# Performance work log

Hardware: AMD Instinct MI355X
Metric: run time of the kernel (lower is better)

The kernel has to match this reference:

```python
import jax, jax.numpy as jnp
import numpy as np

INTER = 256
TEMPERATURE = 4.0
NEG_FILL = -1e9


def setup_inputs() -> dict:
    key = jax.random.key(0)
    ks = jax.random.split(key, 8)
    B, C, H, W = 8, 512, 64, 64
    x_query = jax.random.normal(ks[0], (B, C, H, W), dtype=jnp.float32)
    x_support = jax.random.normal(ks[1], (B, C, H, W), dtype=jnp.float32)
    support_embedding = jax.random.normal(ks[2], (B, INTER, H, W), dtype=jnp.float32)
    support_mask = jax.random.randint(ks[3], (B, 1, H, W), 0, 2).astype(jnp.float32)
    scale = 1.0 / np.sqrt(C)
    theta_w = jax.random.normal(ks[4], (INTER, C), dtype=jnp.float32) * scale
    theta_b = jax.random.normal(ks[5], (INTER,), dtype=jnp.float32) * 0.01
    phi_w = jax.random.normal(ks[6], (INTER, C), dtype=jnp.float32) * scale
    phi_b = jax.random.normal(ks[7], (INTER,), dtype=jnp.float32) * 0.01
    return {
        "x_query": x_query,
        "x_support": x_support,
        "support_embedding": support_embedding,
        "support_mask": support_mask,
        "theta_w": theta_w,
        "theta_b": theta_b,
        "phi_w": phi_w,
        "phi_b": phi_b,
    }


def reference(x_query, x_support, support_embedding, support_mask, theta_w, theta_b, phi_w, phi_b):
    B, C, H, W = x_query.shape
    N = H * W
    # g_x: [B, N, 256]
    g_x = support_embedding.reshape(B, INTER, N).transpose(0, 2, 1)
    # 1x1 convs == per-pixel linear over channels
    theta_x = jnp.einsum('oc,bcn->bno', theta_w, x_query.reshape(B, C, N)) + theta_b  # [B, N, 256]
    phi_x = jnp.einsum('oc,bcn->bon', phi_w, x_support.reshape(B, C, N)) + phi_b[None, :, None]  # [B, 256, N]
    f = jnp.matmul(theta_x, phi_x)  # [B, N, N]
    mask = support_mask.reshape(B, 1, N)
    f = f * mask
    # equality-based mask fill (matches torch masked_fill(f == 0, -1e9))
    f = jnp.where(f == 0, NEG_FILL, f) / TEMPERATURE
    attn = jax.nn.softmax(f, axis=-1)  # dropout is identity in eval mode
    y = jnp.matmul(attn, g_x)  # [B, N, 256]
    y = y.transpose(0, 2, 1).reshape(B, INTER, H, W)
    return y
```

## Files before the change

kernel.cpp:

```cpp
#include <hip/hip_runtime.h>
#include <hip/hip_fp16.h>
#include <stdint.h>

typedef _Float16 f16x8 __attribute__((ext_vector_type(8)));
typedef _Float16 f16x4 __attribute__((ext_vector_type(4)));
typedef float    f32x4 __attribute__((ext_vector_type(4)));

#define MFMA16(a, b, c) __builtin_amdgcn_mfma_f32_16x16x32_f16(a, b, c, 0, 0, 0)

static constexpr int BN   = 8;
static constexpr int CIN  = 512;
static constexpr int NHW  = 4096;
static constexpr int OD   = 256;
static constexpr int KBLK = 32;

#define RSWZ(row, cb) ((((row) << 7)) + ((cb) ^ (((row) & 7) << 4)))

__device__ __forceinline__ f16x8 cvt8(const float4 a, const float4 b) {
    f16x8 r;
    r[0] = (_Float16)a.x; r[1] = (_Float16)a.y; r[2] = (_Float16)a.z; r[3] = (_Float16)a.w;
    r[4] = (_Float16)b.x; r[5] = (_Float16)b.y; r[6] = (_Float16)b.z; r[7] = (_Float16)b.w;
    return r;
}

__device__ __forceinline__ uint32_t pkh2(float x, float y) {
    union { _Float16 h[2]; uint32_t u; } z;
    z.h[0] = (_Float16)x; z.h[1] = (_Float16)y;
    return z.u;
}

__global__ __launch_bounds__(256)
void setup(const float* __restrict__ thw, const float* __restrict__ phw,
           _Float16* __restrict__ wf,
           const float* __restrict__ mask, int* __restrict__ idx,
           int* __restrict__ pos, int* __restrict__ nbArr)
{
    __shared__ int cnt[256];
    __shared__ int pre[257];
    const int t = threadIdx.x;

    if (blockIdx.x < 128) {
        const int i = blockIdx.x * 256 + t;
        const float4 a = ((const float4*)thw)[i];
        const float4 b = ((const float4*)phw)[i];
        f16x4 ra, rb;
        ra[0] = (_Float16)a.x; ra[1] = (_Float16)a.y; ra[2] = (_Float16)a.z; ra[3] = (_Float16)a.w;
        rb[0] = (_Float16)b.x; rb[1] = (_Float16)b.y; rb[2] = (_Float16)b.z; rb[3] = (_Float16)b.w;
        *(f16x4*)(wf + (size_t)i * 4)          = ra;
        *(f16x4*)(wf + 131072 + (size_t)i * 4) = rb;
        return;
    }

    const int b = blockIdx.x - 128;
    const float* mb = mask + (size_t)b * NHW;
    const int base = t * 16;
    float mv[16];
    int c = 0;
    #pragma unroll
    for (int i = 0; i < 16; ++i) { mv[i] = mb[base + i]; c += (mv[i] != 0.0f); }
    cnt[t] = c;
    __syncthreads();
    if (t == 0) {
        int s = 0;
        for (int i = 0; i < 256; ++i) { pre[i] = s; s += cnt[i]; }
        pre[256] = s;
    }
    __syncthreads();
    int o = pre[t];
    #pragma unroll
    for (int i = 0; i < 16; ++i) {
        if (mv[i] != 0.0f) {
            idx[(size_t)b * NHW + o] = base + i;
            pos[(size_t)b * NHW + base + i] = o;
            ++o;
        } else {
            pos[(size_t)b * NHW + base + i] = -1;
        }
    }
    const int Nb = pre[256];
    const int Npad = (Nb + 63) & ~63;
    for (int k = Nb + t; k < Npad; k += 256) idx[(size_t)b * NHW + k] = 0;
    if (t == 0) { nbArr[b * 2] = Nb; nbArr[b * 2 + 1] = Npad >> 5; }
}

__global__ __launch_bounds__(256)
void prep_gather(const float* __restrict__ xq, const float* __restrict__ xs,
                 const _Float16* __restrict__ wf,
                 const float* __restrict__ thb, const float* __restrict__ phb,
                 const int* __restrict__ pos,
                 const float* __restrict__ emb, const int* __restrict__ idx,
                 const int* __restrict__ nbArr,
                 _Float16* __restrict__ Qws, _Float16* __restrict__ Kc,
                 _Float16* __restrict__ Vc)
{
    __shared__ __align__(16) char Xs[64 * 128];
    __shared__ __align__(16) char Ws[256 * 128];
    __shared__ int Ps[64];
    __shared__ int sidx[64];

    const int t    = threadIdx.x;
    const int z    = blockIdx.y;

    if (z >= 16) {
        const int b = z - 16, k0 = blockIdx.x * 64;
        const int Nb = nbArr[b * 2];
        const int Npad = (Nb + 63) & ~63;
        if (k0 >= Npad) return;
        if (t < 64) sidx[t] = idx[(size_t)b * NHW + k0 + t];
        __syncthreads();
        const float* eb = emb + (size_t)b * OD * NHW;
        char* VcB = (char*)(Vc + (size_t)b * OD * NHW);
        #pragma unroll
        for (int r = 0; r < 8; ++r) {
            const int u = r * 256 + t;
            const int o = u >> 3, uc = u & 7;
            const int chunk = uc >> 2, uin = uc & 3;
            float4 a, c;
            #pragma unroll
            for (int i = 0; i < 4; ++i) ((float*)&a)[i] = eb[(size_t)o * NHW + sidx[uc * 8 + i]];
            #pragma unroll
            for (int i = 0; i < 4; ++i) ((float*)&c)[i] = eb[(size_t)o * NHW + sidx[uc * 8 + 4 + i]];
            const f16x8 v = cvt8(a, c);
            *(f16x8*)(VcB + (size_t)o * (NHW * 2) + (size_t)k0 * 2 + chunk * 64
                          + ((uin ^ ((o >> 1) & 3)) * 16)) = v;
        }
        return;
    }

    const int nt = blockIdx.x;
    const int b = z >> 1, sel = z & 1;
    const float* x        = (sel ? xs : xq) + (size_t)b * CIN * NHW;
    const _Float16* w     = wf + (size_t)sel * (OD * CIN);
    const float* bias     = sel ? phb : thb;
    const int n0 = nt * 64;

    const int lane = t & 63, wave = t >> 6;
    const int l16  = lane & 15, lh = lane >> 4;

    if (sel && t < 64) Ps[t] = pos[(size_t)b * NHW + n0 + t];

    f32x4 acc[4][4] = {};

    for (int c0 = 0; c0 < CIN; c0 += 64) {
        #pragma unroll
        for (int rep = 0; rep < 4; ++rep) {
            const int ci = rep * 16 + (t >> 4);
            const int nl = (t & 15) * 4;
            const float4 v = *(const float4*)&x[(size_t)(c0 + ci) * NHW + n0 + nl];
            *(_Float16*)(Xs + RSWZ(nl + 0, ci * 2)) = (_Float16)v.x;
            *(_Float16*)(Xs + RSWZ(nl + 1, ci * 2)) = (_Float16)v.y;
            *(_Float16*)(Xs + RSWZ(nl + 2, ci * 2)) = (_Float16)v.z;
            *(_Float16*)(Xs + RSWZ(nl + 3, ci * 2)) = (_Float16)v.w;
        }
        #pragma unroll
        for (int r = 0; r < 8; ++r) {
            const int u = r * 256 + t;
            const int o = u >> 3, cs8 = (u & 7) * 8;
            const f16x8 v = *(const f16x8*)(w + (size_t)o * CIN + c0 + cs8);
            *(f16x8*)(Ws + RSWZ(o, cs8 * 2)) = v;
        }
        __syncthreads();

        #pragma unroll
        for (int kk = 0; kk < 2; ++kk) {
            f16x8 af[4];
            #pragma unroll
            for (int oo = 0; oo < 4; ++oo)
                af[oo] = *(const f16x8*)(Ws + RSWZ(wave * 64 + oo * 16 + l16, kk * 64 + lh * 16));
            #pragma unroll
            for (int nn = 0; nn < 4; ++nn) {
                const f16x8 bf = *(const f16x8*)(Xs + RSWZ(nn * 16 + l16, kk * 64 + lh * 16));
                #pragma unroll
                for (int oo = 0; oo < 4; ++oo)
                    acc[oo][nn] = MFMA16(af[oo], bf, acc[oo][nn]);
            }
        }
        __syncthreads();
    }

    if (!sel) {
        _Float16* out = Qws + (size_t)b * NHW * OD;
        #pragma unroll
        for (int oo = 0; oo < 4; ++oo) {
            const float4 bi = *(const float4*)&bias[wave * 64 + oo * 16 + lh * 4];
            #pragma unroll
            for (int nn = 0; nn < 4; ++nn) {
                f16x4 v;
                v[0] = (_Float16)(acc[oo][nn][0] + bi.x);
                v[1] = (_Float16)(acc[oo][nn][1] + bi.y);
                v[2] = (_Float16)(acc[oo][nn][2] + bi.z);
                v[3] = (_Float16)(acc[oo][nn][3] + bi.w);
                const int n = n0 + nn * 16 + l16;
                *(f16x4*)&out[(size_t)n * OD + wave * 64 + oo * 16 + lh * 4] = v;
            }
        }
    } else {
        char* KcB = (char*)(Kc + (size_t)b * NHW * OD);
        #pragma unroll
        for (int oo = 0; oo < 4; ++oo) {
            const float4 bi = *(const float4*)&bias[wave * 64 + oo * 16 + lh * 4];
            const int o = wave * 64 + oo * 16 + lh * 4;
            #pragma unroll
            for (int nn = 0; nn < 4; ++nn) {
                const int k = Ps[nn * 16 + l16];
                if (k >= 0) {
                    f16x4 v;
                    v[0] = (_Float16)(acc[oo][nn][0] + bi.x);
                    v[1] = (_Float16)(acc[oo][nn][1] + bi.y);
                    v[2] = (_Float16)(acc[oo][nn][2] + bi.z);
                    v[3] = (_Float16)(acc[oo][nn][3] + bi.w);
                    *(f16x4*)(KcB + (size_t)k * 512
                              + (((o >> 3) * 16) ^ ((k & 7) << 4))
                              + ((o >> 2) & 1) * 8) = v;
                }
            }
        }
    }
}

__device__ __forceinline__ void stage_dma(const char* __restrict__ Kb,
                                          const char* __restrict__ Vb,
                                          int j, int t, int wbase,
                                          char* Kld, char* Vld)
{
    typedef __attribute__((address_space(1))) const unsigned int gu32;
    typedef __attribute__((address_space(3))) unsigned int lu32;
    const char* kb = Kb + (size_t)j * (KBLK * 512);
    #pragma unroll
    for (int r = 0; r < 2; ++r) {
        __builtin_amdgcn_global_load_lds(
            (gu32*)(kb + (size_t)(r * 512 + t) * 16),
            (lu32*)(Kld + (r * 512 + wbase) * 16), 16, 0, 0);
    }
    #pragma unroll
    for (int r = 0; r < 2; ++r) {
        const int u = r * 512 + t, o = u >> 2, sl = u & 3;
        __builtin_amdgcn_global_load_lds(
            (gu32*)(Vb + (size_t)o * (NHW * 2) + (size_t)j * 64 + sl * 16),
            (lu32*)(Vld + (r * 512 + wbase) * 16), 16, 0, 0);
    }
}

__global__ __launch_bounds__(512, 2)
void flash_attn(const _Float16* __restrict__ Qws, const _Float16* __restrict__ Kc,
                const _Float16* __restrict__ Vc, const int* __restrict__ nbArr,
                _Float16* __restrict__ Op0, _Float16* __restrict__ Op1,
                float* __restrict__ Sarr)
{
    const int bid = blockIdx.x;
    const int b = bid & 7, u = bid >> 3;
    const int qt = u >> 1, half = u & 1;
    const int t = threadIdx.x, lane = t & 63, wave = t >> 6;
    const int l16 = lane & 15, lh = lane >> 4;
    const int wbase = wave << 6;

    __shared__ __align__(16) char Kl[2][KBLK * 512];
    __shared__ __align__(16) char Vl[2][OD * 64];

    const _Float16* Qb = Qws + (size_t)b * NHW * OD;
    const char* Kb = (const char*)(Kc + (size_t)b * NHW * OD);
    const char* Vb = (const char*)(Vc + (size_t)b * OD * NHW);
    const int Nb = nbArr[b * 2];
    const int nt = nbArr[b * 2 + 1];
    const int nth = (nt + 1) >> 1;
    const int j0 = half ? nth : 0;
    const int j1 = half ? nt : nth;
    const int nl = j1 - j0;

    f16x8 qf[8][2];
    #pragma unroll
    for (int g = 0; g < 2; ++g) {
        const _Float16* qrow = Qb
            + (size_t)(qt * 256 + wave * 32 + g * 16 + l16) * OD + lh * 8;
        #pragma unroll
        for (int kk = 0; kk < 8; ++kk) qf[kk][g] = *(const f16x8*)(qrow + kk * 32);
    }

    f32x4 accO[16][2] = {};
    float M0 = -INFINITY, L0 = 0.f;
    float M1 = -INFINITY, L1 = 0.f;

    stage_dma(Kb, Vb, j0, t, wbase, Kl[0], Vl[0]);
    __syncthreads();

    #pragma unroll 1
    for (int i = 0; i < nl; ++i) {
        const int jt = j0 + i;
        const int cur = i & 1;
        if (i + 1 < nl) stage_dma(Kb, Vb, jt + 1, t, wbase, Kl[cur ^ 1], Vl[cur ^ 1]);

        f32x4 S[2][2] = {};
        __builtin_amdgcn_s_setprio(1);
        #pragma unroll
        for (int ct = 0; ct < 2; ++ct) {
            const int row = ct * 16 + l16;
            #pragma unroll
            for (int kk = 0; kk < 8; ++kk) {
                const f16x8 kf = *(const f16x8*)(Kl[cur] + row * 512
                                     + ((kk * 64 + lh * 16) ^ ((row & 7) << 4)));
                S[ct][0] = MFMA16(kf, qf[kk][0], S[ct][0]);
                S[ct][1] = MFMA16(kf, qf[kk][1], S[ct][1]);
            }
        }
        __builtin_amdgcn_s_setprio(0);

        const bool tail = (jt * 32 + 32 > Nb);
        float lg[8][2];
        #pragma unroll
        for (int ct = 0; ct < 2; ++ct)
            #pragma unroll
            for (int r = 0; r < 4; ++r) {
                float v0 = S[ct][0][r] * 0.25f;
                float v1 = S[ct][1][r] * 0.25f;
                if (tail) {
                    const int kg = jt * 32 + ct * 16 + lh * 4 + r;
                    if (kg >= Nb) { v0 = -1e30f; v1 = -1e30f; }
                }
                lg[ct * 4 + r][0] = v0;
                lg[ct * 4 + r][1] = v1;
            }

        float m80 = lg[0][0], m81 = lg[0][1];
        #pragma unroll
        for (int i2 = 1; i2 < 8; ++i2) { m80 = fmaxf(m80, lg[i2][0]); m81 = fmaxf(m81, lg[i2][1]); }
        m80 = fmaxf(m80, __shfl_xor(m80, 16));
        m80 = fmaxf(m80, __shfl_xor(m80, 32));
        m81 = fmaxf(m81, __shfl_xor(m81, 16));
        m81 = fmaxf(m81, __shfl_xor(m81, 32));

        if (__any((m80 > M0 + 8.0f) || (m81 > M1 + 8.0f))) {
            const float nm0 = fmaxf(M0, m80), nm1 = fmaxf(M1, m81);
            const float f0 = __expf(M0 - nm0), f1 = __expf(M1 - nm1);
            M0 = nm0; L0 *= f0; M1 = nm1; L1 *= f1;
            #pragma unroll
            for (int oo = 0; oo < 16; ++oo)
                #pragma unroll
                for (int r = 0; r < 4; ++r) {
                    accO[oo][0][r] *= f0;
                    accO[oo][1][r] *= f1;
                }
        }

        float s0 = 0.f, s1 = 0.f;
        #pragma unroll
        for (int i2 = 0; i2 < 8; ++i2) {
            lg[i2][0] = __expf(lg[i2][0] - M0); s0 += lg[i2][0];
            lg[i2][1] = __expf(lg[i2][1] - M1); s1 += lg[i2][1];
        }
        s0 += __shfl_xor(s0, 16); s0 += __shfl_xor(s0, 32); L0 += s0;
        s1 += __shfl_xor(s1, 16); s1 += __shfl_xor(s1, 32); L1 += s1;

        const int src0 = l16 + (((2 * lh) & 3) << 4);
        const int src1 = src0 + 16;
        const bool hi = (lh & 2) != 0;
        f16x8 pf[2];
        #pragma unroll
        for (int g = 0; g < 2; ++g) {
            const uint32_t ps0 = pkh2(lg[0][g], lg[1][g]), ps1 = pkh2(lg[2][g], lg[3][g]);
            const uint32_t ps2 = pkh2(lg[4][g], lg[5][g]), ps3 = pkh2(lg[6][g], lg[7][g]);
            const uint32_t a0 = __shfl(ps0, src0), a2 = __shfl(ps2, src0);
            const uint32_t a1 = __shfl(ps1, src0), a3 = __shfl(ps3, src0);
            const uint32_t b0 = __shfl(ps0, src1), b2 = __shfl(ps2, src1);
            const uint32_t b1 = __shfl(ps1, src1), b3 = __shfl(ps3, src1);
            union { uint32_t u[4]; f16x8 v; } pu;
            pu.u[0] = hi ? a2 : a0;
            pu.u[1] = hi ? a3 : a1;
            pu.u[2] = hi ? b2 : b0;
            pu.u[3] = hi ? b3 : b1;
            pf[g] = pu.v;
        }

        __builtin_amdgcn_s_setprio(1);
        #pragma unroll
        for (int oo = 0; oo < 16; ++oo) {
            const int o = oo * 16 + l16;
            const f16x8 vf = *(const f16x8*)(Vl[cur] + o * 64
                                 + ((lh * 16) ^ (((o >> 1) & 3) << 4)));
            accO[oo][0] = MFMA16(vf, pf[0], accO[oo][0]);
            accO[oo][1] = MFMA16(vf, pf[1], accO[oo][1]);
        }
        __builtin_amdgcn_s_setprio(0);
        __syncthreads();
    }

    _Float16* Od = half ? Op1 : Op0;
    float*    Sd = Sarr + (size_t)half * (BN * NHW) + (size_t)b * NHW;
    const float rl0 = 1.0f / fmaxf(L0, 1e-30f);
    const float rl1 = 1.0f / fmaxf(L1, 1e-30f);
    const int n0 = qt * 256 + wave * 32 + l16;
    if (lh == 0) {
        Sd[n0]      = (L0 > 0.f) ? (M0 + __logf(L0)) : -1e30f;
        Sd[n0 + 16] = (L1 > 0.f) ? (M1 + __logf(L1)) : -1e30f;
    }
    #pragma unroll
    for (int oo = 0; oo < 16; ++oo) {
        #pragma unroll
        for (int r = 0; r < 4; ++r) {
            const int o = oo * 16 + lh * 4 + r;
            _Float16* row = Od + ((size_t)b * OD + o) * NHW;
            row[n0]      = (_Float16)(accO[oo][0][r] * rl0);
            row[n0 + 16] = (_Float16)(accO[oo][1][r] * rl1);
        }
    }
}

__global__ __launch_bounds__(256)
void combine(const _Float16* __restrict__ Op0, const _Float16* __restrict__ Op1,
             const float* __restrict__ Sarr, float* __restrict__ outp)
{
    const int b = blockIdx.y;
    const int n0 = blockIdx.x * 64;
    const int t = threadIdx.x;
    const int nc = n0 + (t & 7) * 8;
    const int ob = t >> 3;
    const float* S0 = Sarr + (size_t)b * NHW;
    const float* S1 = Sarr + (size_t)BN * NHW + (size_t)b * NHW;

    float a0[8], a1[8];
    #pragma unroll
    for (int i = 0; i < 8; ++i) {
        const float s0 = S0[nc + i], s1 = S1[nc + i];
        const float sm = fmaxf(s0, s1);
        const float w0 = __expf(s0 - sm), w1 = __expf(s1 - sm);
        const float inv = 1.0f / (w0 + w1);
        a0[i] = w0 * inv; a1[i] = w1 * inv;
    }
    for (int o = ob; o < OD; o += 32) {
        const size_t base = ((size_t)b * OD + o) * NHW + nc;
        const f16x8 u = *(const f16x8*)(Op0 + base);
        const f16x8 v = *(const f16x8*)(Op1 + base);
        float4 r0, r1;
        r0.x = a0[0] * (float)u[0] + a1[0] * (float)v[0];
        r0.y = a0[1] * (float)u[1] + a1[1] * (float)v[1];
        r0.z = a0[2] * (float)u[2] + a1[2] * (float)v[2];
        r0.w = a0[3] * (float)u[3] + a1[3] * (float)v[3];
        r1.x = a0[4] * (float)u[4] + a1[4] * (float)v[4];
        r1.y = a0[5] * (float)u[5] + a1[5] * (float)v[5];
        r1.z = a0[6] * (float)u[6] + a1[6] * (float)v[6];
        r1.w = a0[7] * (float)u[7] + a1[7] * (float)v[7];
        *(float4*)&outp[base]     = r0;
        *(float4*)&outp[base + 4] = r1;
    }
}

extern "C" void kernel_launch(void* const* d_in, const int* in_sizes, int n_in,
                              void* d_out, int out_size, void* d_ws, size_t ws_size,
                              hipStream_t stream) {
    const float* xq   = (const float*)d_in[0];
    const float* xs   = (const float*)d_in[1];
    const float* emb  = (const float*)d_in[2];
    const float* mask = (const float*)d_in[3];
    const float* thw  = (const float*)d_in[4];
    const float* thb  = (const float*)d_in[5];
    const float* phw  = (const float*)d_in[6];
    const float* phb  = (const float*)d_in[7];
    float* out = (float*)d_out;

    const size_t szT = (size_t)BN * NHW * OD;
    _Float16* Qws = (_Float16*)d_ws;
    _Float16* Op0 = Qws + szT;
    _Float16* Kc  = Op0 + szT;
    _Float16* Vc  = Kc + szT;
    _Float16* wf  = Vc + szT;
    int* idxArr   = (int*)(wf + 2 * OD * CIN);
    int* nbArr    = idxArr + (size_t)BN * NHW;
    int* posArr   = nbArr + 16;
    _Float16* Op1 = (_Float16*)(posArr + (size_t)BN * NHW);
    float* Sarr   = (float*)(Op1 + szT);

    setup<<<dim3(136), 256, 0, stream>>>(thw, phw, wf, mask, idxArr, posArr, nbArr);
    prep_gather<<<dim3(64, 24), 256, 0, stream>>>(xq, xs, wf, thb, phb, posArr,
                                                  emb, idxArr, nbArr, Qws, Kc, Vc);
    flash_attn<<<dim3(256), 512, 0, stream>>>(Qws, Kc, Vc, nbArr, Op0, Op1, Sarr);
    combine<<<dim3(64, BN), 256, 0, stream>>>(Op0, Op1, Sarr, out);
}
```

Measured before the change: 183.0 us.

## Fuse split-KV combine into flash attention via last-block atomic counter

Removes the separate combine kernel launch. The two halves of each query tile now increment a per-tile flag with an atomic after a threadfence, and the second block to finish merges both partial outputs using their log-sum-exp values and writes the final fp32 output. The flags are zeroed in the setup kernel. This saves a launch and lets the combine overlap with other blocks' attention work, but the merge now falls on whichever block finishes last and adds fence and atomic overhead.

```diff
diff --git a/kernel.cpp b/kernel.cpp
--- a/kernel.cpp
+++ b/kernel.cpp
@@ -33,7 +33,8 @@
 void setup(const float* __restrict__ thw, const float* __restrict__ phw,
            _Float16* __restrict__ wf,
            const float* __restrict__ mask, int* __restrict__ idx,
-           int* __restrict__ pos, int* __restrict__ nbArr)
+           int* __restrict__ pos, int* __restrict__ nbArr,
+           int* __restrict__ flags)
 {
     __shared__ int cnt[256];
     __shared__ int pre[257];
@@ -52,6 +53,7 @@
     }
 
     const int b = blockIdx.x - 128;
+    if (t < 16) flags[b * 16 + t] = 0;
     const float* mb = mask + (size_t)b * NHW;
     const int base = t * 16;
     float mv[16];
@@ -245,7 +247,8 @@
 void flash_attn(const _Float16* __restrict__ Qws, const _Float16* __restrict__ Kc,
                 const _Float16* __restrict__ Vc, const int* __restrict__ nbArr,
                 _Float16* __restrict__ Op0, _Float16* __restrict__ Op1,
-                float* __restrict__ Sarr)
+                float* __restrict__ Sarr, int* __restrict__ flags,
+                float* __restrict__ outp)
 {
     const int bid = blockIdx.x;
     const int b = bid & 7, u = bid >> 3;
@@ -256,6 +259,7 @@
 
     __shared__ __align__(16) char Kl[2][KBLK * 512];
     __shared__ __align__(16) char Vl[2][OD * 64];
+    __shared__ int sflag;
 
     const _Float16* Qb = Qws + (size_t)b * NHW * OD;
     const char* Kb = (const char*)(Kc + (size_t)b * NHW * OD);
@@ -402,44 +406,42 @@
             row[n0 + 16] = (_Float16)(accO[oo][1][r] * rl1);
         }
     }
-}
-
-__global__ __launch_bounds__(256)
-void combine(const _Float16* __restrict__ Op0, const _Float16* __restrict__ Op1,
-             const float* __restrict__ Sarr, float* __restrict__ outp)
-{
-    const int b = blockIdx.y;
-    const int n0 = blockIdx.x * 64;
-    const int t = threadIdx.x;
-    const int nc = n0 + (t & 7) * 8;
-    const int ob = t >> 3;
-    const float* S0 = Sarr + (size_t)b * NHW;
-    const float* S1 = Sarr + (size_t)BN * NHW + (size_t)b * NHW;
-
-    float a0[8], a1[8];
-    #pragma unroll
-    for (int i = 0; i < 8; ++i) {
-        const float s0 = S0[nc + i], s1 = S1[nc + i];
-        const float sm = fmaxf(s0, s1);
-        const float w0 = __expf(s0 - sm), w1 = __expf(s1 - sm);
-        const float inv = 1.0f / (w0 + w1);
-        a0[i] = w0 * inv; a1[i] = w1 * inv;
-    }
-    for (int o = ob; o < OD; o += 32) {
-        const size_t base = ((size_t)b * OD + o) * NHW + nc;
-        const f16x8 u = *(const f16x8*)(Op0 + base);
-        const f16x8 v = *(const f16x8*)(Op1 + base);
-        float4 r0, r1;
-        r0.x = a0[0] * (float)u[0] + a1[0] * (float)v[0];
-        r0.y = a0[1] * (float)u[1] + a1[1] * (float)v[1];
-        r0.z = a0[2] * (float)u[2] + a1[2] * (float)v[2];
-        r0.w = a0[3] * (float)u[3] + a1[3] * (float)v[3];
-        r1.x = a0[4] * (float)u[4] + a1[4] * (float)v[4];
-        r1.y = a0[5] * (float)u[5] + a1[5] * (float)v[5];
-        r1.z = a0[6] * (float)u[6] + a1[6] * (float)v[6];
-        r1.w = a0[7] * (float)u[7] + a1[7] * (float)v[7];
-        *(float4*)&outp[base]     = r0;
-        *(float4*)&outp[base + 4] = r1;
+
+    __threadfence();
+    __syncthreads();
+    if (t == 0) sflag = atomicAdd(&flags[b * 16 + qt], 1);
+    __syncthreads();
+    if (sflag == 1) {
+        __threadfence();
+        const float* S0 = Sarr + (size_t)b * NHW;
+        const float* S1 = Sarr + (size_t)BN * NHW + (size_t)b * NHW;
+        const int nc = qt * 256 + (t & 31) * 8;
+        const int ob = t >> 5;
+        float a0[8], a1[8];
+        #pragma unroll
+        for (int i = 0; i < 8; ++i) {
+            const float s0 = S0[nc + i], s1 = S1[nc + i];
+            const float sm = fmaxf(s0, s1);
+            const float w0 = __expf(s0 - sm), w1 = __expf(s1 - sm);
+            const float inv = 1.0f / (w0 + w1);
+            a0[i] = w0 * inv; a1[i] = w1 * inv;
+        }
+        for (int o = ob; o < OD; o += 16) {
+            const size_t base = ((size_t)b * OD + o) * NHW + nc;
+            const f16x8 uu = *(const f16x8*)(Op0 + base);
+            const f16x8 vv = *(const f16x8*)(Op1 + base);
+            float4 r0, r1;
+            r0.x = a0[0] * (float)uu[0] + a1[0] * (float)vv[0];
+            r0.y = a0[1] * (float)uu[1] + a1[1] * (float)vv[1];
+            r0.z = a0[2] * (float)uu[2] + a1[2] * (float)vv[2];
+            r0.w = a0[3] * (float)uu[3] + a1[3] * (float)vv[3];
+            r1.x = a0[4] * (float)uu[4] + a1[4] * (float)vv[4];
+            r1.y = a0[5] * (float)uu[5] + a1[5] * (float)vv[5];
+            r1.z = a0[6] * (float)uu[6] + a1[6] * (float)vv[6];
+            r1.w = a0[7] * (float)uu[7] + a1[7] * (float)vv[7];
+            *(float4*)&outp[base]     = r0;
+            *(float4*)&outp[base + 4] = r1;
+        }
     }
 }
 
@@ -467,10 +469,11 @@
     int* posArr   = nbArr + 16;
     _Float16* Op1 = (_Float16*)(posArr + (size_t)BN * NHW);
     float* Sarr   = (float*)(Op1 + szT);
-
-    setup<<<dim3(136), 256, 0, stream>>>(thw, phw, wf, mask, idxArr, posArr, nbArr);
+    int* flags    = (int*)(Sarr + 2 * (size_t)BN * NHW);
+
+    setup<<<dim3(136), 256, 0, stream>>>(thw, phw, wf, mask, idxArr, posArr, nbArr, flags);
     prep_gather<<<dim3(64, 24), 256, 0, stream>>>(xq, xs, wf, thb, phb, posArr,
                                                   emb, idxArr, nbArr, Qws, Kc, Vc);
-    flash_attn<<<dim3(256), 512, 0, stream>>>(Qws, Kc, Vc, nbArr, Op0, Op1, Sarr);
-    combine<<<dim3(64, BN), 256, 0, stream>>>(Op0, Op1, Sarr, out);
-}
+    flash_attn<<<dim3(256), 512, 0, stream>>>(Qws, Kc, Vc, nbArr, Op0, Op1, Sarr,
+                                              flags, out);
+}
```

Measured after the change: 267.0 us. 45.9% more time.
